# Optimization experiments

Measured on AMD Instinct MI355X. Metric: run time of the kernel, lower is better.

## Reference

```python
import jax, jax.numpy as jnp
import numpy as np

N_CELL, N_GENE, D, E = 100000, 20000, 128, 1000000


def setup_inputs() -> dict:
    key = jax.random.key(0)
    ks = jax.random.split(key, 16)
    return {
        "cell_z": jax.random.normal(ks[0], (N_CELL, D), jnp.float32),
        "gene_z": jax.random.normal(ks[1], (N_GENE, D), jnp.float32),
        "W_gene": jax.random.normal(ks[2], (D, D), jnp.float32) / np.sqrt(D),
        "b_gene": jax.random.normal(ks[3], (D,), jnp.float32) * 0.01,
        "cell_scale": jax.random.normal(ks[4], (N_CELL,), jnp.float32),
        "cell_bias": jax.random.normal(ks[5], (N_CELL,), jnp.float32),
        "cell_std": jax.random.uniform(ks[6], (N_CELL,), jnp.float32, 0.1, 1.0),
        "gene_scale": jax.random.normal(ks[7], (N_GENE,), jnp.float32),
        "gene_bias": jax.random.normal(ks[8], (N_GENE,), jnp.float32),
        "gene_std": jax.random.uniform(ks[9], (N_GENE,), jnp.float32, 0.1, 1.0),
        "src_idx": jax.random.randint(ks[10], (E,), 0, N_CELL, jnp.int32),
        "dst_idx": jax.random.randint(ks[11], (E,), 0, N_GENE, jnp.int32),
        "cell_n_id": jax.random.randint(ks[12], (N_CELL,), 0, N_CELL, jnp.int32),
        "gene_n_id": jax.random.randint(ks[13], (N_GENE,), 0, N_GENE, jnp.int32),
    }


def reference(cell_z, gene_z, W_gene, b_gene,
              cell_scale, cell_bias, cell_std,
              gene_scale, gene_bias, gene_std,
              src_idx, dst_idx, cell_n_id, gene_n_id):
    # Relation projection: 'cell' -> Identity, 'gene' -> Linear + LeakyReLU.
    # Project per-node then gather (mathematically identical to the original
    # gather-then-project since projection is pointwise per node).
    gene_proj = jax.nn.leaky_relu(gene_z @ W_gene + b_gene)  # [N_GENE, D]
    u = cell_z[src_idx]            # [E, D] gather of src node embeddings
    v = gene_proj[dst_idx]         # [E, D] gather of projected dst embeddings

    # Per-edge scale/bias/std lookups via global node ids (n_id[edge_index]).
    sid = cell_n_id[src_idx]       # [E]
    did = gene_n_id[dst_idx]       # [E]
    s_sc, s_b, s_sd = cell_scale[sid], cell_bias[sid], cell_std[sid]
    d_sc, d_b, d_sd = gene_scale[did], gene_bias[did], gene_std[did]

    dot = jnp.sum(u * v, axis=-1)  # [E]
    loc = dot * s_sc * d_sc + s_b + d_b
    std = s_sd * d_sd
    return jnp.stack([loc, std])   # [2, E]
```

## Files before the change

kernel.cpp:

```cpp
#include <hip/hip_runtime.h>

#define N_CELL 100000
#define N_GENE 20000
#define DIM    128
#define N_EDGE 1000000

#define NS_STRIPE 20
#define NTILE     40
#define NBLK_SORT 977

#define NB_PROJ 1250
#define NB_HIST 977
#define NB_CTAB 391
#define NB_GTAB 79
#define NB_CAST 6250
#define NB_PREP (NB_PROJ + NB_HIST + NB_CTAB + NB_GTAB + NB_CAST)

typedef float f32x4 __attribute__((ext_vector_type(4)));

__device__ inline unsigned short f2bf(float f) {
    unsigned u = __float_as_uint(f);
    u += 0x7fffu + ((u >> 16) & 1u);
    return (unsigned short)(u >> 16);
}

__device__ inline void dot2(float& acc, unsigned a, unsigned b) {
    asm("v_dot2_f32_bf16 %0, %1, %2, %0" : "+v"(acc) : "v"(a), "v"(b));
}

__device__ inline int tile_of(int s, int d) {
    const int ss = (int)(((unsigned long long)s * 429497ULL) >> 31);
    const int ds = (d >= 10000) ? 1 : 0;
    return ds * NS_STRIPE + ss;
}

__device__ inline unsigned pack_sd(int s, int d) {
    return ((unsigned)s << 15) | (unsigned)d;
}

__global__ __launch_bounds__(256) void prep_kernel(
    const float* __restrict__ gene_z,
    const float* __restrict__ W,
    const float* __restrict__ b,
    ushort* __restrict__ gene_projb,
    const float* __restrict__ cell_z,
    ushort4* __restrict__ cell_zb4,
    const int*   __restrict__ src_idx,
    const int*   __restrict__ dst_idx,
    const int*   __restrict__ cell_n_id,
    const int*   __restrict__ gene_n_id,
    const float* __restrict__ cell_scale,
    const float* __restrict__ cell_bias,
    const float* __restrict__ cell_std,
    const float* __restrict__ gene_scale,
    const float* __restrict__ gene_bias,
    const float* __restrict__ gene_std,
    float4* __restrict__ cell_p4,
    float4* __restrict__ gene_p4,
    int* __restrict__ counts)
{
    __shared__ float zlds[16][DIM];

    const int tid = threadIdx.x;
    int blk = blockIdx.x;

    if (blk < NB_PROJ) {
        const int row0 = blk * 16;
        const f32x4* Z4  = (const f32x4*)(gene_z + (long)row0 * DIM);
        f32x4*       zl4 = (f32x4*)&zlds[0][0];
        zl4[tid]       = Z4[tid];
        zl4[tid + 256] = Z4[tid + 256];
        __syncthreads();

        const int col   = tid & 127;
        const int rbase = (tid >> 7) * 8;

        const float bias = b[col];
        float acc[8];
        #pragma unroll
        for (int r = 0; r < 8; ++r) acc[r] = bias;

        for (int k4 = 0; k4 < DIM / 4; ++k4) {
            const float w0 = W[(k4 * 4 + 0) * DIM + col];
            const float w1 = W[(k4 * 4 + 1) * DIM + col];
            const float w2 = W[(k4 * 4 + 2) * DIM + col];
            const float w3 = W[(k4 * 4 + 3) * DIM + col];
            #pragma unroll
            for (int rp = 0; rp < 4; ++rp) {
                const float4 za = ((const float4*)&zlds[rbase + 2*rp][0])[k4];
                const float4 zb = ((const float4*)&zlds[rbase + 2*rp + 1][0])[k4];
                acc[2*rp]     = fmaf(za.x, w0, fmaf(za.y, w1,
                                fmaf(za.z, w2, fmaf(za.w, w3, acc[2*rp]))));
                acc[2*rp + 1] = fmaf(zb.x, w0, fmaf(zb.y, w1,
                                fmaf(zb.z, w2, fmaf(zb.w, w3, acc[2*rp + 1]))));
            }
        }
        #pragma unroll
        for (int r = 0; r < 8; ++r) {
            const float v = acc[r];
            gene_projb[(long)(row0 + rbase + r) * DIM + col] =
                f2bf(v > 0.f ? v : 0.01f * v);
        }
        return;
    }
    blk -= NB_PROJ;

    if (blk < NB_HIST) {
        if (!counts) return;
        int* lcnt = (int*)&zlds[0][0];
        if (tid < NTILE) lcnt[tid] = 0;
        __syncthreads();
        #pragma unroll
        for (int q = 0; q < 4; ++q) {
            const int e = blk * 1024 + q * 256 + tid;
            if (e < N_EDGE) {
                const int t = tile_of(src_idx[e], dst_idx[e]);
                atomicAdd(&lcnt[t], 1);
            }
        }
        __syncthreads();
        if (tid < NTILE) counts[tid * NBLK_SORT + blk] = lcnt[tid];
        return;
    }
    blk -= NB_HIST;

    if (blk < NB_CTAB) {
        if (!cell_p4) return;
        const int c = blk * 256 + tid;
        if (c < N_CELL) {
            const int id = cell_n_id[c];
            cell_p4[c] = make_float4(cell_scale[id], cell_bias[id],
                                     cell_std[id], 0.f);
        }
        return;
    }
    blk -= NB_CTAB;

    if (blk < NB_GTAB) {
        if (!gene_p4) return;
        const int g = blk * 256 + tid;
        if (g < N_GENE) {
            const int id = gene_n_id[g];
            gene_p4[g] = make_float4(gene_scale[id], gene_bias[id],
                                     gene_std[id], 0.f);
        }
        return;
    }
    blk -= NB_GTAB;

    const f32x4* in4 = (const f32x4*)cell_z;
    const int base = blk * 512 + tid;
    const f32x4 v0 = in4[base];
    const f32x4 v1 = in4[base + 256];
    ushort4 o0, o1;
    o0.x = f2bf(v0.x); o0.y = f2bf(v0.y); o0.z = f2bf(v0.z); o0.w = f2bf(v0.w);
    o1.x = f2bf(v1.x); o1.y = f2bf(v1.y); o1.z = f2bf(v1.z); o1.w = f2bf(v1.w);
    cell_zb4[base]       = o0;
    cell_zb4[base + 256] = o1;
}

__global__ __launch_bounds__(256) void scanA_kernel(
    int* __restrict__ counts, int* __restrict__ totals)
{
    __shared__ int sd[256];
    const int t   = blockIdx.x;
    const int tid = threadIdx.x;
    int carry = 0;
    for (int c = 0; c < 4; ++c) {
        const int idx = c * 256 + tid;
        const int val = (idx < NBLK_SORT) ? counts[t * NBLK_SORT + idx] : 0;
        sd[tid] = val;
        __syncthreads();
        #pragma unroll
        for (int off = 1; off < 256; off <<= 1) {
            const int tmp = (tid >= off) ? sd[tid - off] : 0;
            __syncthreads();
            sd[tid] += tmp;
            __syncthreads();
        }
        const int incl = sd[tid];
        const int ctot = sd[255];
        if (idx < NBLK_SORT) counts[t * NBLK_SORT + idx] = carry + incl - val;
        carry += ctot;
        __syncthreads();
    }
    if (tid == 0) totals[t] = carry;
}

__global__ __launch_bounds__(256) void scatter_kernel(
    const int* __restrict__ src_idx,
    const int* __restrict__ dst_idx,
    const int* __restrict__ counts,
    const int* __restrict__ totals,
    unsigned* __restrict__ sorted_p,
    int*      __restrict__ rank)
{
    __shared__ int lcnt[NTILE];
    __shared__ int sbase[NTILE];
    __shared__ int lbase[NTILE];
    const int tid = threadIdx.x;
    const int blk = blockIdx.x;
    if (tid < NTILE) lcnt[tid] = 0;
    __syncthreads();

    int ts[4], rs[4], ss[4], ds[4];
    #pragma unroll
    for (int c = 0; c < 4; ++c) {
        const int e = blk * 1024 + c * 256 + tid;
        if (e < N_EDGE) {
            ss[c] = src_idx[e];
            ds[c] = dst_idx[e];
            ts[c] = tile_of(ss[c], ds[c]);
            rs[c] = atomicAdd(&lcnt[ts[c]], 1);
        } else { ts[c] = -1; rs[c] = 0; ss[c] = 0; ds[c] = 0; }
    }
    __syncthreads();
    if (tid == 0) {
        int s = 0;
        for (int i = 0; i < NTILE; ++i) { sbase[i] = s; s += totals[i]; }
    }
    __syncthreads();
    if (tid < NTILE) lbase[tid] = sbase[tid] + counts[tid * NBLK_SORT + blk];
    __syncthreads();

    #pragma unroll
    for (int c = 0; c < 4; ++c) {
        const int e = blk * 1024 + c * 256 + tid;
        if (ts[c] >= 0) {
            const int pos = lbase[ts[c]] + rs[c];
            sorted_p[pos] = pack_sd(ss[c], ds[c]);
            rank[e] = pos;
        }
    }
}

__global__ __launch_bounds__(256) void edge_sorted_kernel(
    const ushort* __restrict__ cell_zb,
    const ushort* __restrict__ gene_projb,
    const unsigned* __restrict__ sorted_p,
    const float4* __restrict__ cell_p4,
    const float4* __restrict__ gene_p4,
    float2* __restrict__ res)
{
    const int wg  = blockIdx.x;
    const int xcd = wg & 7;
    const int sub = wg >> 3;
    const int q = 15625 / 8, r = 15625 % 8;
    const int swz = ((xcd < r) ? xcd * (q + 1) : r * (q + 1) + (xcd - r) * q) + sub;

    const int tid  = threadIdx.x;
    const int lane = tid & 15;
    const int grp  = swz * 16 + (tid >> 4);

    const uint4 p = ((const uint4*)sorted_p)[grp];
    const int s0 = (int)(p.x >> 15), d0 = (int)(p.x & 0x7fffu);
    const int s1 = (int)(p.y >> 15), d1 = (int)(p.y & 0x7fffu);
    const int s2 = (int)(p.z >> 15), d2 = (int)(p.z & 0x7fffu);
    const int s3 = (int)(p.w >> 15), d3 = (int)(p.w & 0x7fffu);

    uint4 a0 = ((const uint4*)(cell_zb    + (long)s0 * DIM))[lane];
    uint4 a1 = ((const uint4*)(cell_zb    + (long)s1 * DIM))[lane];
    uint4 a2 = ((const uint4*)(cell_zb    + (long)s2 * DIM))[lane];
    uint4 a3 = ((const uint4*)(cell_zb    + (long)s3 * DIM))[lane];
    uint4 v0 = ((const uint4*)(gene_projb + (long)d0 * DIM))[lane];
    uint4 v1 = ((const uint4*)(gene_projb + (long)d1 * DIM))[lane];
    uint4 v2 = ((const uint4*)(gene_projb + (long)d2 * DIM))[lane];
    uint4 v3 = ((const uint4*)(gene_projb + (long)d3 * DIM))[lane];

    float dot0 = 0.f, dot1 = 0.f, dot2v = 0.f, dot3 = 0.f;
    dot2(dot0, a0.x, v0.x); dot2(dot0, a0.y, v0.y);
    dot2(dot0, a0.z, v0.z); dot2(dot0, a0.w, v0.w);
    dot2(dot1, a1.x, v1.x); dot2(dot1, a1.y, v1.y);
    dot2(dot1, a1.z, v1.z); dot2(dot1, a1.w, v1.w);
    dot2(dot2v, a2.x, v2.x); dot2(dot2v, a2.y, v2.y);
    dot2(dot2v, a2.z, v2.z); dot2(dot2v, a2.w, v2.w);
    dot2(dot3, a3.x, v3.x); dot2(dot3, a3.y, v3.y);
    dot2(dot3, a3.z, v3.z); dot2(dot3, a3.w, v3.w);

    #define RED(d)                 \
        d += __shfl_xor(d, 1);     \
        d += __shfl_xor(d, 2);     \
        d += __shfl_xor(d, 4);     \
        d += __shfl_xor(d, 8);
    RED(dot0) RED(dot1) RED(dot2v) RED(dot3)
    #undef RED

    if (lane < 4) {
        const float dj = (lane & 2) ? ((lane & 1) ? dot3 : dot2v)
                                    : ((lane & 1) ? dot1 : dot0);
        const int sj   = (lane & 2) ? ((lane & 1) ? s3 : s2)
                                    : ((lane & 1) ? s1 : s0);
        const int djx  = (lane & 2) ? ((lane & 1) ? d3 : d2)
                                    : ((lane & 1) ? d1 : d0);
        const float4 cs = cell_p4[sj];
        const float4 gs = gene_p4[djx];
        res[grp * 4 + lane] =
            make_float2(dj * cs.x * gs.x + cs.y + gs.y, cs.z * gs.z);
    }
}

__global__ __launch_bounds__(256) void fixup_kernel(
    const int*    __restrict__ rank,
    const float2* __restrict__ res,
    float* __restrict__ out)
{
    const int e0 = (blockIdx.x * 256 + threadIdx.x) * 4;
    if (e0 >= N_EDGE) return;
    const int4 r4 = *(const int4*)(rank + e0);
    const float2 r0 = res[r4.x];
    const float2 r1 = res[r4.y];
    const float2 r2 = res[r4.z];
    const float2 r3 = res[r4.w];
    *(float4*)(out + e0)          = make_float4(r0.x, r1.x, r2.x, r3.x);
    *(float4*)(out + N_EDGE + e0) = make_float4(r0.y, r1.y, r2.y, r3.y);
}

template<bool TAB>
__global__ __launch_bounds__(256) void edge_kernel(
    const ushort* __restrict__ cell_zb,
    const ushort* __restrict__ gene_projb,
    const int*   __restrict__ src_idx,
    const int*   __restrict__ dst_idx,
    const int*   __restrict__ cell_n_id,
    const int*   __restrict__ gene_n_id,
    const float* __restrict__ cell_scale,
    const float* __restrict__ cell_bias,
    const float* __restrict__ cell_std,
    const float* __restrict__ gene_scale,
    const float* __restrict__ gene_bias,
    const float* __restrict__ gene_std,
    const float4* __restrict__ cell_p4,
    const float4* __restrict__ gene_p4,
    float* __restrict__ out)
{
    const int tid  = threadIdx.x;
    const int lane = tid & 15;
    const int grp  = blockIdx.x * 16 + (tid >> 4);
    const int e0   = grp * 4;

    const int4 s4 = ((const int4*)src_idx)[grp];
    const int4 d4 = ((const int4*)dst_idx)[grp];

    uint4 a0 = ((const uint4*)(cell_zb    + (long)s4.x * DIM))[lane];
    uint4 a1 = ((const uint4*)(cell_zb    + (long)s4.y * DIM))[lane];
    uint4 a2 = ((const uint4*)(cell_zb    + (long)s4.z * DIM))[lane];
    uint4 a3 = ((const uint4*)(cell_zb    + (long)s4.w * DIM))[lane];
    uint4 v0 = ((const uint4*)(gene_projb + (long)d4.x * DIM))[lane];
    uint4 v1 = ((const uint4*)(gene_projb + (long)d4.y * DIM))[lane];
    uint4 v2 = ((const uint4*)(gene_projb + (long)d4.z * DIM))[lane];
    uint4 v3 = ((const uint4*)(gene_projb + (long)d4.w * DIM))[lane];

    float dot0 = 0.f, dot1 = 0.f, dot2v = 0.f, dot3 = 0.f;
    dot2(dot0, a0.x, v0.x); dot2(dot0, a0.y, v0.y);
    dot2(dot0, a0.z, v0.z); dot2(dot0, a0.w, v0.w);
    dot2(dot1, a1.x, v1.x); dot2(dot1, a1.y, v1.y);
    dot2(dot1, a1.z, v1.z); dot2(dot1, a1.w, v1.w);
    dot2(dot2v, a2.x, v2.x); dot2(dot2v, a2.y, v2.y);
    dot2(dot2v, a2.z, v2.z); dot2(dot2v, a2.w, v2.w);
    dot2(dot3, a3.x, v3.x); dot2(dot3, a3.y, v3.y);
    dot2(dot3, a3.z, v3.z); dot2(dot3, a3.w, v3.w);

    #define RED(d)                 \
        d += __shfl_xor(d, 1);     \
        d += __shfl_xor(d, 2);     \
        d += __shfl_xor(d, 4);     \
        d += __shfl_xor(d, 8);
    RED(dot0) RED(dot1) RED(dot2v) RED(dot3)
    #undef RED

    if (lane < 4) {
        const float dj = (lane & 2) ? ((lane & 1) ? dot3 : dot2v)
                                    : ((lane & 1) ? dot1 : dot0);
        const int sj   = (lane & 2) ? ((lane & 1) ? s4.w : s4.z)
                                    : ((lane & 1) ? s4.y : s4.x);
        const int djx  = (lane & 2) ? ((lane & 1) ? d4.w : d4.z)
                                    : ((lane & 1) ? d4.y : d4.x);
        float sc_s, b_s, sd_s, sc_d, b_d, sd_d;
        if (TAB) {
            const float4 cs = cell_p4[sj];
            const float4 gs = gene_p4[djx];
            sc_s = cs.x; b_s = cs.y; sd_s = cs.z;
            sc_d = gs.x; b_d = gs.y; sd_d = gs.z;
        } else {
            const int sid = cell_n_id[sj];
            const int did = gene_n_id[djx];
            sc_s = cell_scale[sid]; b_s = cell_bias[sid]; sd_s = cell_std[sid];
            sc_d = gene_scale[did]; b_d = gene_bias[did]; sd_d = gene_std[did];
        }
        const int e = e0 + lane;
        out[e]          = dj * sc_s * sc_d + b_s + b_d;
        out[N_EDGE + e] = sd_s * sd_d;
    }
}

extern "C" void kernel_launch(void* const* d_in, const int* in_sizes, int n_in,
                              void* d_out, int out_size, void* d_ws, size_t ws_size,
                              hipStream_t stream) {
    const float* cell_z     = (const float*)d_in[0];
    const float* gene_z     = (const float*)d_in[1];
    const float* W_gene     = (const float*)d_in[2];
    const float* b_gene     = (const float*)d_in[3];
    const float* cell_scale = (const float*)d_in[4];
    const float* cell_bias  = (const float*)d_in[5];
    const float* cell_std   = (const float*)d_in[6];
    const float* gene_scale = (const float*)d_in[7];
    const float* gene_bias  = (const float*)d_in[8];
    const float* gene_std   = (const float*)d_in[9];
    const int*   src_idx    = (const int*)d_in[10];
    const int*   dst_idx    = (const int*)d_in[11];
    const int*   cell_n_id  = (const int*)d_in[12];
    const int*   gene_n_id  = (const int*)d_in[13];

    char* ws = (char*)d_ws;
    size_t off = 0;
    ushort* gene_projb = (ushort*)(ws + off); off += (size_t)N_GENE * DIM * 2;
    ushort* cell_zb    = (ushort*)(ws + off); off += (size_t)N_CELL * DIM * 2;
    const size_t base_need = off;

    float4* cell_p4 = nullptr; float4* gene_p4 = nullptr;
    size_t off_tab = off;
    const size_t tab_need = (size_t)N_CELL * 16 + (size_t)N_GENE * 16;

    unsigned* sorted_p = nullptr; int* rank = nullptr; float2* res = nullptr;
    int* counts = nullptr; int* totals = nullptr;
    const size_t sort_need = (size_t)N_EDGE * 4
                           + (size_t)N_EDGE * 4
                           + (size_t)N_EDGE * 8
                           + (size_t)NTILE * NBLK_SORT * 4 + 256;

    const bool tab = (ws_size >= base_need + tab_need);
    const bool srt = tab && (ws_size >= base_need + tab_need + sort_need);

    if (tab) {
        cell_p4 = (float4*)(ws + off_tab);
        gene_p4 = (float4*)(ws + off_tab + (size_t)N_CELL * 16);
        off = off_tab + tab_need;
    }
    if (srt) {
        sorted_p = (unsigned*)(ws + off); off += (size_t)N_EDGE * 4;
        rank     = (int*)(ws + off);      off += (size_t)N_EDGE * 4;
        res      = (float2*)(ws + off);   off += (size_t)N_EDGE * 8;
        counts   = (int*)(ws + off);      off += (size_t)NTILE * NBLK_SORT * 4;
        totals   = (int*)(ws + off);      off += 256;
    }

    float* out = (float*)d_out;

    prep_kernel<<<NB_PREP, 256, 0, stream>>>(
        gene_z, W_gene, b_gene, gene_projb,
        cell_z, (ushort4*)cell_zb,
        src_idx, dst_idx, cell_n_id, gene_n_id,
        cell_scale, cell_bias, cell_std,
        gene_scale, gene_bias, gene_std,
        cell_p4, gene_p4, counts);

    if (srt) {
        scanA_kernel<<<NTILE, 256, 0, stream>>>(counts, totals);
        scatter_kernel<<<NBLK_SORT, 256, 0, stream>>>(
            src_idx, dst_idx, counts, totals, sorted_p, rank);
        edge_sorted_kernel<<<N_EDGE / 64, 256, 0, stream>>>(
            cell_zb, gene_projb, sorted_p, cell_p4, gene_p4, res);
        fixup_kernel<<<(N_EDGE / 4 + 255) / 256, 256, 0, stream>>>(rank, res, out);
    } else if (tab) {
        edge_kernel<true><<<N_EDGE / 64, 256, 0, stream>>>(
            cell_zb, gene_projb, src_idx, dst_idx, cell_n_id, gene_n_id,
            cell_scale, cell_bias, cell_std, gene_scale, gene_bias, gene_std,
            cell_p4, gene_p4, out);
    } else {
        edge_kernel<false><<<N_EDGE / 64, 256, 0, stream>>>(
            cell_zb, gene_projb, src_idx, dst_idx, cell_n_id, gene_n_id,
            cell_scale, cell_bias, cell_std, gene_scale, gene_bias, gene_std,
            nullptr, nullptr, out);
    }
}
```

Baseline: 85.93 us.

## Split prep kernel and compute gene projection with bf16 dot2 on transposed weights

The single fused prep kernel becomes four launches: misc (W cast and transpose to bf16 plus the per-node parameter tables), histogram, projection and cell_z cast. The projection now casts gene_z to bf16 in LDS and accumulates with v_dot2_f32_bf16 over a swizzled, transposed bf16 W in LDS, computing a 4x4 register tile per thread over 32 rows per block instead of fp32 FMAs. This is meant to cut the projection's ALU and LDS cost. It adds three kernel launches and serializes work that previously shared one grid, and rounding the projection inputs to bf16 lowers accuracy.

```diff
diff --git a/kernel.cpp b/kernel.cpp
--- a/kernel.cpp
+++ b/kernel.cpp
@@ -9,12 +9,14 @@
 #define NTILE     40
 #define NBLK_SORT 977
 
-#define NB_PROJ 1250
-#define NB_HIST 977
-#define NB_CTAB 391
-#define NB_GTAB 79
-#define NB_CAST 6250
-#define NB_PREP (NB_PROJ + NB_HIST + NB_CTAB + NB_GTAB + NB_CAST)
+#define NB_WCAST 8
+#define NB_CTAB  391
+#define NB_GTAB  79
+#define NB_MISC  (NB_WCAST + NB_CTAB + NB_GTAB)
+
+#define NB_PROJ  625
+#define NB_HIST  977
+#define NB_CAST  6250
 
 typedef float f32x4 __attribute__((ext_vector_type(4)));
 
@@ -38,15 +40,11 @@
     return ((unsigned)s << 15) | (unsigned)d;
 }
 
-__global__ __launch_bounds__(256) void prep_kernel(
-    const float* __restrict__ gene_z,
+__device__ inline float lrelu(float v) { return v > 0.f ? v : 0.01f * v; }
+
+__global__ __launch_bounds__(256) void misc_kernel(
     const float* __restrict__ W,
-    const float* __restrict__ b,
-    ushort* __restrict__ gene_projb,
-    const float* __restrict__ cell_z,
-    ushort4* __restrict__ cell_zb4,
-    const int*   __restrict__ src_idx,
-    const int*   __restrict__ dst_idx,
+    ushort* __restrict__ Wbt,
     const int*   __restrict__ cell_n_id,
     const int*   __restrict__ gene_n_id,
     const float* __restrict__ cell_scale,
@@ -56,73 +54,28 @@
     const float* __restrict__ gene_bias,
     const float* __restrict__ gene_std,
     float4* __restrict__ cell_p4,
-    float4* __restrict__ gene_p4,
-    int* __restrict__ counts)
-{
-    __shared__ float zlds[16][DIM];
-
+    float4* __restrict__ gene_p4)
+{
     const int tid = threadIdx.x;
     int blk = blockIdx.x;
 
-    if (blk < NB_PROJ) {
-        const int row0 = blk * 16;
-        const f32x4* Z4  = (const f32x4*)(gene_z + (long)row0 * DIM);
-        f32x4*       zl4 = (f32x4*)&zlds[0][0];
-        zl4[tid]       = Z4[tid];
-        zl4[tid + 256] = Z4[tid + 256];
-        __syncthreads();
-
-        const int col   = tid & 127;
-        const int rbase = (tid >> 7) * 8;
-
-        const float bias = b[col];
-        float acc[8];
+    if (blk < NB_WCAST) {
+        const int t   = blk * 256 + tid;
+        const int col = t >> 4;
+        const int k8  = t & 15;
+        unsigned short w[8];
         #pragma unroll
-        for (int r = 0; r < 8; ++r) acc[r] = bias;
-
-        for (int k4 = 0; k4 < DIM / 4; ++k4) {
-            const float w0 = W[(k4 * 4 + 0) * DIM + col];
-            const float w1 = W[(k4 * 4 + 1) * DIM + col];
-            const float w2 = W[(k4 * 4 + 2) * DIM + col];
-            const float w3 = W[(k4 * 4 + 3) * DIM + col];
-            #pragma unroll
-            for (int rp = 0; rp < 4; ++rp) {
-                const float4 za = ((const float4*)&zlds[rbase + 2*rp][0])[k4];
-                const float4 zb = ((const float4*)&zlds[rbase + 2*rp + 1][0])[k4];
-                acc[2*rp]     = fmaf(za.x, w0, fmaf(za.y, w1,
-                                fmaf(za.z, w2, fmaf(za.w, w3, acc[2*rp]))));
-                acc[2*rp + 1] = fmaf(zb.x, w0, fmaf(zb.y, w1,
-                                fmaf(zb.z, w2, fmaf(zb.w, w3, acc[2*rp + 1]))));
-            }
-        }
-        #pragma unroll
-        for (int r = 0; r < 8; ++r) {
-            const float v = acc[r];
-            gene_projb[(long)(row0 + rbase + r) * DIM + col] =
-                f2bf(v > 0.f ? v : 0.01f * v);
-        }
+        for (int j = 0; j < 8; ++j)
+            w[j] = f2bf(W[(k8 * 8 + j) * DIM + col]);
+        uint4 o;
+        o.x = (unsigned)w[0] | ((unsigned)w[1] << 16);
+        o.y = (unsigned)w[2] | ((unsigned)w[3] << 16);
+        o.z = (unsigned)w[4] | ((unsigned)w[5] << 16);
+        o.w = (unsigned)w[6] | ((unsigned)w[7] << 16);
+        ((uint4*)Wbt)[t] = o;
         return;
     }
-    blk -= NB_PROJ;
-
-    if (blk < NB_HIST) {
-        if (!counts) return;
-        int* lcnt = (int*)&zlds[0][0];
-        if (tid < NTILE) lcnt[tid] = 0;
-        __syncthreads();
-        #pragma unroll
-        for (int q = 0; q < 4; ++q) {
-            const int e = blk * 1024 + q * 256 + tid;
-            if (e < N_EDGE) {
-                const int t = tile_of(src_idx[e], dst_idx[e]);
-                atomicAdd(&lcnt[t], 1);
-            }
-        }
-        __syncthreads();
-        if (tid < NTILE) counts[tid * NBLK_SORT + blk] = lcnt[tid];
-        return;
-    }
-    blk -= NB_HIST;
+    blk -= NB_WCAST;
 
     if (blk < NB_CTAB) {
         if (!cell_p4) return;
@@ -136,20 +89,117 @@
     }
     blk -= NB_CTAB;
 
-    if (blk < NB_GTAB) {
-        if (!gene_p4) return;
-        const int g = blk * 256 + tid;
-        if (g < N_GENE) {
-            const int id = gene_n_id[g];
-            gene_p4[g] = make_float4(gene_scale[id], gene_bias[id],
-                                     gene_std[id], 0.f);
+    if (!gene_p4) return;
+    const int g = blk * 256 + tid;
+    if (g < N_GENE) {
+        const int id = gene_n_id[g];
+        gene_p4[g] = make_float4(gene_scale[id], gene_bias[id],
+                                 gene_std[id], 0.f);
+    }
+}
+
+__global__ __launch_bounds__(256) void proj_kernel(
+    const float* __restrict__ gene_z,
+    const float* __restrict__ b,
+    const ushort* __restrict__ Wbt,
+    ushort* __restrict__ gene_projb)
+{
+    __shared__ ushort zb[32 * DIM];
+    __shared__ uint4  wl[2048];
+
+    const int tid = threadIdx.x;
+
+    const uint4* wg = (const uint4*)Wbt;
+    #pragma unroll
+    for (int i = 0; i < 8; ++i) {
+        const int u = i * 256 + tid;
+        const int c = u >> 4, j = u & 15;
+        wl[(c << 4) | (j ^ (c & 15))] = wg[u];
+    }
+
+    const int row0 = blockIdx.x * 32;
+    const f32x4* Z4 = (const f32x4*)(gene_z + (long)row0 * DIM);
+    #pragma unroll
+    for (int i = 0; i < 4; ++i) {
+        const int idx = i * 256 + tid;
+        const f32x4 v = Z4[idx];
+        ushort4 o;
+        o.x = f2bf(v.x); o.y = f2bf(v.y); o.z = f2bf(v.z); o.w = f2bf(v.w);
+        ((ushort4*)zb)[idx] = o;
+    }
+    __syncthreads();
+
+    const int cg = tid & 31;
+    const int rg = tid >> 5;
+
+    const float4 bb = ((const float4*)b)[cg];
+    float acc[4][4];
+    #pragma unroll
+    for (int r = 0; r < 4; ++r) {
+        acc[r][0] = bb.x; acc[r][1] = bb.y; acc[r][2] = bb.z; acc[r][3] = bb.w;
+    }
+
+    const uint4* zr = (const uint4*)zb;
+    #pragma unroll 4
+    for (int k8 = 0; k8 < 16; ++k8) {
+        uint4 z[4], w[4];
+        #pragma unroll
+        for (int r = 0; r < 4; ++r)
+            z[r] = zr[(rg * 4 + r) * 16 + k8];
+        #pragma unroll
+        for (int c = 0; c < 4; ++c) {
+            const int col = cg * 4 + c;
+            w[c] = wl[(col << 4) | (k8 ^ (col & 15))];
         }
-        return;
-    }
-    blk -= NB_GTAB;
-
+        #pragma unroll
+        for (int r = 0; r < 4; ++r)
+            #pragma unroll
+            for (int c = 0; c < 4; ++c) {
+                dot2(acc[r][c], z[r].x, w[c].x);
+                dot2(acc[r][c], z[r].y, w[c].y);
+                dot2(acc[r][c], z[r].z, w[c].z);
+                dot2(acc[r][c], z[r].w, w[c].w);
+            }
+    }
+
+    #pragma unroll
+    for (int r = 0; r < 4; ++r) {
+        ushort4 o;
+        o.x = f2bf(lrelu(acc[r][0]));
+        o.y = f2bf(lrelu(acc[r][1]));
+        o.z = f2bf(lrelu(acc[r][2]));
+        o.w = f2bf(lrelu(acc[r][3]));
+        *(ushort4*)(gene_projb + (long)(row0 + rg * 4 + r) * DIM + cg * 4) = o;
+    }
+}
+
+__global__ __launch_bounds__(256) void hist_kernel(
+    const int* __restrict__ src_idx,
+    const int* __restrict__ dst_idx,
+    int* __restrict__ counts)
+{
+    __shared__ int lcnt[NTILE];
+    const int tid = threadIdx.x;
+    const int blk = blockIdx.x;
+    if (tid < NTILE) lcnt[tid] = 0;
+    __syncthreads();
+    #pragma unroll
+    for (int q = 0; q < 4; ++q) {
+        const int e = blk * 1024 + q * 256 + tid;
+        if (e < N_EDGE) {
+            const int t = tile_of(src_idx[e], dst_idx[e]);
+            atomicAdd(&lcnt[t], 1);
+        }
+    }
+    __syncthreads();
+    if (tid < NTILE) counts[tid * NBLK_SORT + blk] = lcnt[tid];
+}
+
+__global__ __launch_bounds__(256) void cast_kernel(
+    const float* __restrict__ cell_z, ushort4* __restrict__ cell_zb4)
+{
     const f32x4* in4 = (const f32x4*)cell_z;
-    const int base = blk * 512 + tid;
+    const int base = blockIdx.x * 512 + threadIdx.x;
     const f32x4 v0 = in4[base];
     const f32x4 v1 = in4[base + 256];
     ushort4 o0, o1;
@@ -415,6 +465,7 @@
     size_t off = 0;
     ushort* gene_projb = (ushort*)(ws + off); off += (size_t)N_GENE * DIM * 2;
     ushort* cell_zb    = (ushort*)(ws + off); off += (size_t)N_CELL * DIM * 2;
+    ushort* Wbt        = (ushort*)(ws + off); off += (size_t)DIM * DIM * 2;
     const size_t base_need = off;
 
     float4* cell_p4 = nullptr; float4* gene_p4 = nullptr;
@@ -423,8 +474,7 @@
 
     unsigned* sorted_p = nullptr; int* rank = nullptr; float2* res = nullptr;
     int* counts = nullptr; int* totals = nullptr;
-    const size_t sort_need = (size_t)N_EDGE * 4
-                           + (size_t)N_EDGE * 4
+    const size_t sort_need = (size_t)N_EDGE * 4 + (size_t)N_EDGE * 4
                            + (size_t)N_EDGE * 8
                            + (size_t)NTILE * NBLK_SORT * 4 + 256;
 
@@ -446,13 +496,14 @@
 
     float* out = (float*)d_out;
 
-    prep_kernel<<<NB_PREP, 256, 0, stream>>>(
-        gene_z, W_gene, b_gene, gene_projb,
-        cell_z, (ushort4*)cell_zb,
-        src_idx, dst_idx, cell_n_id, gene_n_id,
+    misc_kernel<<<NB_MISC, 256, 0, stream>>>(
+        W_gene, Wbt, cell_n_id, gene_n_id,
         cell_scale, cell_bias, cell_std,
-        gene_scale, gene_bias, gene_std,
-        cell_p4, gene_p4, counts);
+        gene_scale, gene_bias, gene_std, cell_p4, gene_p4);
+    if (srt)
+        hist_kernel<<<NB_HIST, 256, 0, stream>>>(src_idx, dst_idx, counts);
+    proj_kernel<<<NB_PROJ, 256, 0, stream>>>(gene_z, b_gene, Wbt, gene_projb);
+    cast_kernel<<<NB_CAST, 256, 0, stream>>>(cell_z, (ushort4*)cell_zb);
 
     if (srt) {
         scanA_kernel<<<NTILE, 256, 0, stream>>>(counts, totals);
```

After: 90.48 us. 5.3% more time.
